# Kernel optimization log

Hardware: AMD Instinct MI355X
Metric: run time of the kernel (lower is better)

## Reference

```python
import jax, jax.numpy as jnp
import numpy as np

E, M, IN, OUT = 8, 8192, 2048, 8192


def setup_inputs() -> dict:
    key = jax.random.key(0)
    k1, k2, k3 = jax.random.split(key, 3)
    inputs = jax.random.normal(k1, (M, IN), dtype=jnp.float32)
    # truncated_normal(-3,3) scaled by init_scale/sqrt(In), matching MoELinear.init
    weight = jax.random.truncated_normal(k2, -3.0, 3.0, (E, IN, OUT), dtype=jnp.float32) * (1.0 / np.sqrt(IN))
    bias = jax.random.normal(k3, (OUT,), dtype=jnp.float32) * 0.02
    # tokens are pre-sorted by expert; balanced routing: M/E tokens per expert
    group_sizes = jnp.full((E,), M // E, dtype=jnp.int32)
    return {"inputs": inputs, "weight": weight, "group_sizes": group_sizes, "bias": bias}


def _ragged_matmul(inputs, weight, group_sizes):
    """Grouped GEMM: out[m] = inputs[m] @ weight[expert_of(m)].

    Tokens are contiguous per expert; group_sizes[e] gives the count for
    expert e. Same math as jax.lax.ragged_dot / megablox gmm.
    """
    n_experts = weight.shape[0]
    m = inputs.shape[0]
    # static-length repeat -> per-token expert id, jit-safe
    expert_ids = jnp.repeat(jnp.arange(n_experts, dtype=group_sizes.dtype),
                            group_sizes, total_repeat_length=m)  # [M]

    def body(acc, ew):
        e, w = ew  # w: [In, Out]
        mask = (expert_ids == e).astype(inputs.dtype)  # [M]
        return acc + (inputs * mask[:, None]) @ w, None

    acc0 = jnp.zeros((m, weight.shape[2]), dtype=inputs.dtype)
    out, _ = jax.lax.scan(body, acc0, (jnp.arange(n_experts, dtype=group_sizes.dtype), weight))
    return out


def reference(inputs, weight, group_sizes, bias):
    # MoELinear.__call__ (ragged_dot path): grouped matmul + bias
    return _ragged_matmul(inputs, weight, group_sizes) + bias
```

## Files before the change

### kernel.cpp

```cpp
#include <hip/hip_runtime.h>
#include <stdint.h>

#define E_ 8
#define M_ 8192
#define K_ 2048
#define N_ 8192

#define BM 256
#define BN 256
#define BK 64
#define NT (K_ / BK)
#define LDS_BYTES 131072

typedef __attribute__((ext_vector_type(8))) short bf16x8;
typedef __attribute__((ext_vector_type(4))) float f32x4;
typedef __attribute__((ext_vector_type(8))) unsigned short us8;

__device__ __forceinline__ unsigned short f2bf(float f) {
  union { float f; uint32_t u; } v; v.f = f;
  uint32_t u = v.u;
  uint32_t r = (u + 0x7FFFu + ((u >> 16) & 1u)) >> 16;
  return (unsigned short)r;
}

__device__ __forceinline__ void gload_lds16(const void* g, void* l) {
  __builtin_amdgcn_global_load_lds(
      (const __attribute__((address_space(1))) unsigned int*)g,
      (__attribute__((address_space(3))) unsigned int*)l,
      16, 0, 0);
}

__global__ __launch_bounds__(256) void conv_a(const float* __restrict__ A,
                                              unsigned short* __restrict__ Ab,
                                              int n8) {
  int stride = gridDim.x * blockDim.x;
  for (int idx = blockIdx.x * blockDim.x + threadIdx.x; idx < n8; idx += stride) {
    const float4* p = reinterpret_cast<const float4*>(A) + (size_t)idx * 2;
    float4 x0 = p[0], x1 = p[1];
    us8 o;
    o[0] = f2bf(x0.x); o[1] = f2bf(x0.y); o[2] = f2bf(x0.z); o[3] = f2bf(x0.w);
    o[4] = f2bf(x1.x); o[5] = f2bf(x1.y); o[6] = f2bf(x1.z); o[7] = f2bf(x1.w);
    *reinterpret_cast<us8*>(Ab + (size_t)idx * 8) = o;
  }
}

__global__ __launch_bounds__(256) void conv_wT(const float* __restrict__ W,
                                               unsigned short* __restrict__ Wt,
                                               int e_fixed) {
  __shared__ float t[64][65];
  int tid = threadIdx.x;
  int tx = tid & 63, ty = tid >> 6;
  int n0 = blockIdx.x * 64, k0 = blockIdx.y * 64;
  int e = (gridDim.z > 1) ? blockIdx.z : e_fixed;
  size_t win = (size_t)e * K_ * N_;
  size_t wout = (gridDim.z > 1) ? win : 0;

  #pragma unroll
  for (int r = 0; r < 16; ++r) {
    int kl = r * 4 + ty;
    t[kl][tx] = W[win + (size_t)(k0 + kl) * N_ + n0 + tx];
  }
  __syncthreads();
  int px = tid & 31, py = tid >> 5;
  #pragma unroll
  for (int r = 0; r < 8; ++r) {
    int nl = r * 8 + py;
    unsigned int pack = (unsigned int)f2bf(t[2 * px][nl]) |
                        ((unsigned int)f2bf(t[2 * px + 1][nl]) << 16);
    *reinterpret_cast<unsigned int*>(Wt + wout + (size_t)(n0 + nl) * K_ + k0 + 2 * px) = pack;
  }
}

__global__ __launch_bounds__(512, 2) void moe_gemm_bf16(
    const unsigned short* __restrict__ Ab,
    const unsigned short* __restrict__ Wt,
    const int* __restrict__ gs,
    const float* __restrict__ bias,
    float* __restrict__ C,
    int only_expert, size_t wt_stride) {
  extern __shared__ char smem[];

  int tile_n = blockIdx.x;
  int tile_m = blockIdx.y;

  int expert = -1, row_start = 0, rows = 0;
  if (only_expert >= 0) {
    int off = 0;
    for (int e = 0; e < only_expert; ++e) off += gs[e];
    int g = gs[only_expert];
    int t0 = tile_m * BM;
    if (t0 >= g) return;
    expert = only_expert;
    row_start = off + t0;
    rows = min(BM, g - t0);
  } else {
    int acc = 0, off = 0;
    for (int e = 0; e < E_; ++e) {
      int g = gs[e];
      int t = (g + BM - 1) / BM;
      if (expert < 0 && tile_m < acc + t) {
        int lt = tile_m - acc;
        expert = e;
        row_start = off + lt * BM;
        rows = min(BM, g - lt * BM);
      }
      acc += t;
      off += g;
    }
    if (expert < 0) return;
  }

  const unsigned short* WtE = Wt + (size_t)expert * wt_stride;

  int tid = threadIdx.x;
  int lane = tid & 63;
  int wave = tid >> 6;
  int wr = wave >> 2;
  int wc = wave & 3;
  int bh = wc >> 1;
  int ln15 = lane & 15;
  int n0 = tile_n * BN;

  int slot0 = (((lane >> 4) ^ (ln15 & 7)) << 4);
  int aBase = wr * 16384 + ln15 * 128;
  int bBase = 32768 + bh * 16384 + (wc & 1) * 8192 + ln15 * 128;

  int soff = tid * 16;
  int crow = tid >> 3;
  int lslot = (tid & 7) ^ (crow & 7);
  int scol = lslot * 8;

  const unsigned short* aS[4];
  const unsigned short* bS[4];
  #pragma unroll
  for (int c = 0; c < 4; ++c) {
    int r = c * 64 + crow;
    int gr = r < rows ? r : 0;
    aS[c] = Ab + (size_t)(row_start + gr) * K_ + scol;
    bS[c] = WtE + (size_t)(n0 + r) * K_ + scol;
  }

#define STG_A(DB, c, kt) \
  gload_lds16(aS[c] + (kt) * 64, smem + (DB) + (c) * 8192 + soff)
#define STG_B(DB, c, kt) \
  gload_lds16(bS[c] + (kt) * 64, smem + (DB) + 32768 + (c) * 8192 + soff)

  f32x4 acc4[8][4];
  #pragma unroll
  for (int i = 0; i < 8; ++i)
    #pragma unroll
    for (int j = 0; j < 4; ++j)
      acc4[i][j] = f32x4{0.f, 0.f, 0.f, 0.f};

#define DS_A(frag, DB, MH, KS)                                                \
  _Pragma("unroll") for (int mi = 0; mi < 4; ++mi)                            \
    frag[mi] = *(const bf16x8*)(smem + (DB) + aBase + (MH) * 8192 +           \
                                mi * 2048 + (slot0 ^ ((KS) << 6)));
#define DS_B(frag, DB, KS)                                                    \
  _Pragma("unroll") for (int nj = 0; nj < 4; ++nj)                            \
    frag[nj] = *(const bf16x8*)(smem + (DB) + bBase + nj * 2048 +             \
                                (slot0 ^ ((KS) << 6)));
#define MFMA16(MB, af, bf)                                                    \
  __builtin_amdgcn_s_setprio(1);                                              \
  _Pragma("unroll") for (int mi = 0; mi < 4; ++mi)                            \
    _Pragma("unroll") for (int nj = 0; nj < 4; ++nj)                          \
      acc4[(MB) + mi][nj] = __builtin_amdgcn_mfma_f32_16x16x32_bf16(          \
          af[mi], bf[nj], acc4[(MB) + mi][nj], 0, 0, 0);                      \
  __builtin_amdgcn_s_setprio(0);

#define TILE4(DB, DBN, KTN)                                                   \
  do {                                                                        \
    bf16x8 af[4], bf[4];                                                      \
                                                \
    DS_A(af, DB, 0, 0); DS_B(bf, DB, 0);                                      \
    STG_A(DBN, 0, KTN); STG_A(DBN, 2, KTN); STG_B(DBN, 0, KTN);               \
    __builtin_amdgcn_s_barrier();                                             \
    asm volatile("s_waitcnt lgkmcnt(0)" ::: "memory");                        \
    __builtin_amdgcn_sched_barrier(0);                                        \
    MFMA16(0, af, bf);                                                        \
    asm volatile("s_waitcnt vmcnt(3)" ::: "memory");                          \
    __builtin_amdgcn_s_barrier();                                             \
                             \
    DS_A(af, DB, 1, 0);                                                       \
    STG_B(DBN, 1, KTN); STG_B(DBN, 2, KTN); STG_B(DBN, 3, KTN);               \
    __builtin_amdgcn_s_barrier();                                             \
    asm volatile("s_waitcnt lgkmcnt(0)" ::: "memory");                        \
    __builtin_amdgcn_sched_barrier(0);                                        \
    MFMA16(4, af, bf);                                                        \
    __builtin_amdgcn_s_barrier();                                             \
                                                   \
    DS_A(af, DB, 0, 1); DS_B(bf, DB, 1);                                      \
    STG_A(DBN, 1, KTN); STG_A(DBN, 3, KTN);                                   \
    __builtin_amdgcn_s_barrier();                                             \
    asm volatile("s_waitcnt lgkmcnt(0)" ::: "memory");                        \
    __builtin_amdgcn_sched_barrier(0);                                        \
    MFMA16(0, af, bf);                                                        \
    __builtin_amdgcn_s_barrier();                                             \
                                                            \
    DS_A(af, DB, 1, 1);                                                       \
    __builtin_amdgcn_s_barrier();                                             \
    asm volatile("s_waitcnt lgkmcnt(0)" ::: "memory");                        \
    __builtin_amdgcn_sched_barrier(0);                                        \
    MFMA16(4, af, bf);                                                        \
    asm volatile("s_waitcnt vmcnt(2)" ::: "memory");                          \
    __builtin_amdgcn_s_barrier();                                             \
  } while (0)

  STG_B(0, 0, 0); STG_B(0, 1, 0); STG_B(0, 2, 0); STG_B(0, 3, 0);
  STG_A(0, 0, 0); STG_A(0, 2, 0);
  STG_A(0, 1, 0); STG_A(0, 3, 0);
  asm volatile("s_waitcnt vmcnt(2)" ::: "memory");
  __builtin_amdgcn_s_barrier();

  for (int t2 = 0; t2 < NT; t2 += 2) {
    int k2 = (t2 + 2 >= NT) ? 0 : t2 + 2;
    TILE4(0, 65536, t2 + 1);
    TILE4(65536, 0, k2);
  }
#undef TILE4
#undef DS_A
#undef DS_B
#undef MFMA16
#undef STG_A
#undef STG_B

  asm volatile("s_waitcnt vmcnt(0)" ::: "memory");

  float bv[4];
  #pragma unroll
  for (int nj = 0; nj < 4; ++nj) bv[nj] = bias[n0 + wc * 64 + nj * 16 + ln15];
  #pragma unroll
  for (int mi = 0; mi < 8; ++mi) {
    int r0 = wr * 128 + mi * 16 + (lane >> 4) * 4;
    #pragma unroll
    for (int r = 0; r < 4; ++r) {
      int lr = r0 + r;
      if (lr < rows) {
        float* Cp = C + (size_t)(row_start + lr) * N_ + n0 + wc * 64 + ln15;
        #pragma unroll
        for (int nj = 0; nj < 4; ++nj) Cp[nj * 16] = acc4[mi][nj][r] + bv[nj];
      }
    }
  }
}

__global__ __launch_bounds__(256) void moe_naive(const float* __restrict__ A,
                                                 const float* __restrict__ W,
                                                 const int* __restrict__ gs,
                                                 const float* __restrict__ bias,
                                                 float* __restrict__ C) {
  int col = blockIdx.x * 16 + (threadIdx.x & 15);
  int row = blockIdx.y * 16 + (threadIdx.x >> 4);
  int acc = 0, e = E_ - 1;
  for (int i = 0; i < E_; ++i) {
    int g = gs[i];
    if (row >= acc && row < acc + g) { e = i; break; }
    acc += g;
  }
  const float* a = A + (size_t)row * K_;
  const float* w = W + (size_t)e * K_ * N_ + col;
  float s = 0.f;
  for (int k = 0; k < K_; ++k) s += a[k] * w[(size_t)k * N_];
  C[(size_t)row * N_ + col] = s + bias[col];
}

extern "C" void kernel_launch(void* const* d_in, const int* in_sizes, int n_in,
                              void* d_out, int out_size, void* d_ws, size_t ws_size,
                              hipStream_t stream) {
  const float* A = (const float*)d_in[0];
  const float* W = (const float*)d_in[1];
  const int* gs = (const int*)d_in[2];
  const float* bias = (const float*)d_in[3];
  float* C = (float*)d_out;

  const size_t needA = (size_t)M_ * K_ * 2;
  const size_t needWall = (size_t)E_ * K_ * N_ * 2;
  const size_t needW1 = (size_t)K_ * N_ * 2;

  (void)hipFuncSetAttribute((const void*)moe_gemm_bf16,
                            hipFuncAttributeMaxDynamicSharedMemorySize, LDS_BYTES);

  if (ws_size >= needA + needWall) {
    unsigned short* Abf = (unsigned short*)d_ws;
    unsigned short* Wtb = (unsigned short*)((char*)d_ws + needA);
    conv_a<<<2048, 256, 0, stream>>>(A, Abf, (M_ * K_) / 8);
    dim3 gw(N_ / 64, K_ / 64, E_);
    conv_wT<<<gw, 256, 0, stream>>>(W, Wtb, 0);
    dim3 gg(N_ / BN, M_ / BM + E_);
    moe_gemm_bf16<<<gg, 512, LDS_BYTES, stream>>>(Abf, Wtb, gs, bias, C, -1, (size_t)N_ * K_);
  } else if (ws_size >= needA + needW1) {
    unsigned short* Abf = (unsigned short*)d_ws;
    unsigned short* Wtb = (unsigned short*)((char*)d_ws + needA);
    conv_a<<<2048, 256, 0, stream>>>(A, Abf, (M_ * K_) / 8);
    for (int e = 0; e < E_; ++e) {
      dim3 gw(N_ / 64, K_ / 64, 1);
      conv_wT<<<gw, 256, 0, stream>>>(W, Wtb, e);
      dim3 gg(N_ / BN, M_ / BM);
      moe_gemm_bf16<<<gg, 512, LDS_BYTES, stream>>>(Abf, Wtb, gs, bias, C, e, 0);
    }
  } else {
    dim3 gn(N_ / 16, M_ / 16);
    moe_naive<<<gn, 256, 0, stream>>>(A, W, gs, bias, C);
  }
}
```

Baseline: 431.2 us.

## Shrink GEMM tile to 128x128 with 4 waves and simplified pipeline

Reduces the block tile from 256x256 to 128x128, uses 256 threads and half the LDS, and each wave now owns a 64x64 output. Global-to-LDS staging is issued all at once per k-step and drained with a full vmcnt wait, replacing the staggered partial waits. The aim is higher occupancy and more blocks in the grid. In exchange, operand reuse per loaded byte drops and load latency is less hidden.

```diff
diff --git a/kernel.cpp b/kernel.cpp
--- a/kernel.cpp
+++ b/kernel.cpp
@@ -6,11 +6,12 @@
 #define K_ 2048
 #define N_ 8192
 
-#define BM 256
-#define BN 256
+#define BM 128
+#define BN 128
 #define BK 64
 #define NT (K_ / BK)
-#define LDS_BYTES 131072
+#define TILE_B 32768
+#define LDS_BYTES 65536
 
 typedef __attribute__((ext_vector_type(8))) short bf16x8;
 typedef __attribute__((ext_vector_type(4))) float f32x4;
@@ -71,7 +72,7 @@
   }
 }
 
-__global__ __launch_bounds__(512, 2) void moe_gemm_bf16(
+__global__ __launch_bounds__(256, 2) void moe_gemm_bf16(
     const unsigned short* __restrict__ Ab,
     const unsigned short* __restrict__ Wt,
     const int* __restrict__ gs,
@@ -115,15 +116,14 @@
   int tid = threadIdx.x;
   int lane = tid & 63;
   int wave = tid >> 6;
-  int wr = wave >> 2;
-  int wc = wave & 3;
-  int bh = wc >> 1;
+  int wr = wave >> 1;
+  int wc = wave & 1;
   int ln15 = lane & 15;
   int n0 = tile_n * BN;
 
   int slot0 = (((lane >> 4) ^ (ln15 & 7)) << 4);
-  int aBase = wr * 16384 + ln15 * 128;
-  int bBase = 32768 + bh * 16384 + (wc & 1) * 8192 + ln15 * 128;
+  int aBase = wr * 8192 + ln15 * 128;
+  int bBase = 16384 + wc * 8192 + ln15 * 128;
 
   int soff = tid * 16;
   int crow = tid >> 3;
@@ -134,104 +134,89 @@
   const unsigned short* bS[4];
   #pragma unroll
   for (int c = 0; c < 4; ++c) {
-    int r = c * 64 + crow;
+    int r = c * 32 + crow;
     int gr = r < rows ? r : 0;
     aS[c] = Ab + (size_t)(row_start + gr) * K_ + scol;
     bS[c] = WtE + (size_t)(n0 + r) * K_ + scol;
   }
 
 #define STG_A(DB, c, kt) \
-  gload_lds16(aS[c] + (kt) * 64, smem + (DB) + (c) * 8192 + soff)
+  gload_lds16(aS[c] + (kt) * 64, smem + (DB) + (c) * 4096 + soff)
 #define STG_B(DB, c, kt) \
-  gload_lds16(bS[c] + (kt) * 64, smem + (DB) + 32768 + (c) * 8192 + soff)
-
-  f32x4 acc4[8][4];
-  #pragma unroll
-  for (int i = 0; i < 8; ++i)
+  gload_lds16(bS[c] + (kt) * 64, smem + (DB) + 16384 + (c) * 4096 + soff)
+#define STG_ALL(DB, kt)                                                       \
+  do {                                                                        \
+    STG_B(DB, 0, kt); STG_B(DB, 1, kt); STG_B(DB, 2, kt); STG_B(DB, 3, kt);   \
+    STG_A(DB, 0, kt); STG_A(DB, 1, kt); STG_A(DB, 2, kt); STG_A(DB, 3, kt);   \
+  } while (0)
+
+  f32x4 acc4[4][4];
+  #pragma unroll
+  for (int i = 0; i < 4; ++i)
     #pragma unroll
     for (int j = 0; j < 4; ++j)
       acc4[i][j] = f32x4{0.f, 0.f, 0.f, 0.f};
 
-#define DS_A(frag, DB, MH, KS)                                                \
+#define DS_A(frag, DB, KS)                                                    \
   _Pragma("unroll") for (int mi = 0; mi < 4; ++mi)                            \
-    frag[mi] = *(const bf16x8*)(smem + (DB) + aBase + (MH) * 8192 +           \
-                                mi * 2048 + (slot0 ^ ((KS) << 6)));
+    frag[mi] = *(const bf16x8*)(smem + (DB) + aBase + mi * 2048 +             \
+                                (slot0 ^ ((KS) << 6)));
 #define DS_B(frag, DB, KS)                                                    \
   _Pragma("unroll") for (int nj = 0; nj < 4; ++nj)                            \
     frag[nj] = *(const bf16x8*)(smem + (DB) + bBase + nj * 2048 +             \
                                 (slot0 ^ ((KS) << 6)));
-#define MFMA16(MB, af, bf)                                                    \
+#define MFMA16(af, bf)                                                        \
   __builtin_amdgcn_s_setprio(1);                                              \
   _Pragma("unroll") for (int mi = 0; mi < 4; ++mi)                            \
     _Pragma("unroll") for (int nj = 0; nj < 4; ++nj)                          \
-      acc4[(MB) + mi][nj] = __builtin_amdgcn_mfma_f32_16x16x32_bf16(          \
-          af[mi], bf[nj], acc4[(MB) + mi][nj], 0, 0, 0);                      \
+      acc4[mi][nj] = __builtin_amdgcn_mfma_f32_16x16x32_bf16(                 \
+          af[mi], bf[nj], acc4[mi][nj], 0, 0, 0);                             \
   __builtin_amdgcn_s_setprio(0);
 
-#define TILE4(DB, DBN, KTN)                                                   \
+#define TILE2(DB, DBN, KTN)                                                   \
   do {                                                                        \
     bf16x8 af[4], bf[4];                                                      \
-                                                \
-    DS_A(af, DB, 0, 0); DS_B(bf, DB, 0);                                      \
-    STG_A(DBN, 0, KTN); STG_A(DBN, 2, KTN); STG_B(DBN, 0, KTN);               \
+                                                                      \
+    DS_A(af, DB, 0); DS_B(bf, DB, 0);                                         \
+    STG_ALL(DBN, KTN);                                                        \
     __builtin_amdgcn_s_barrier();                                             \
     asm volatile("s_waitcnt lgkmcnt(0)" ::: "memory");                        \
     __builtin_amdgcn_sched_barrier(0);                                        \
-    MFMA16(0, af, bf);                                                        \
-    asm volatile("s_waitcnt vmcnt(3)" ::: "memory");                          \
-    __builtin_amdgcn_s_barrier();                                             \
-                             \
-    DS_A(af, DB, 1, 0);                                                       \
-    STG_B(DBN, 1, KTN); STG_B(DBN, 2, KTN); STG_B(DBN, 3, KTN);               \
+    MFMA16(af, bf);                                                           \
+    __builtin_amdgcn_s_barrier();                                             \
+                                                                      \
+    DS_A(af, DB, 1); DS_B(bf, DB, 1);                                         \
     __builtin_amdgcn_s_barrier();                                             \
     asm volatile("s_waitcnt lgkmcnt(0)" ::: "memory");                        \
     __builtin_amdgcn_sched_barrier(0);                                        \
-    MFMA16(4, af, bf);                                                        \
-    __builtin_amdgcn_s_barrier();                                             \
-                                                   \
-    DS_A(af, DB, 0, 1); DS_B(bf, DB, 1);                                      \
-    STG_A(DBN, 1, KTN); STG_A(DBN, 3, KTN);                                   \
-    __builtin_amdgcn_s_barrier();                                             \
-    asm volatile("s_waitcnt lgkmcnt(0)" ::: "memory");                        \
-    __builtin_amdgcn_sched_barrier(0);                                        \
-    MFMA16(0, af, bf);                                                        \
-    __builtin_amdgcn_s_barrier();                                             \
-                                                            \
-    DS_A(af, DB, 1, 1);                                                       \
-    __builtin_amdgcn_s_barrier();                                             \
-    asm volatile("s_waitcnt lgkmcnt(0)" ::: "memory");                        \
-    __builtin_amdgcn_sched_barrier(0);                                        \
-    MFMA16(4, af, bf);                                                        \
-    asm volatile("s_waitcnt vmcnt(2)" ::: "memory");                          \
+    MFMA16(af, bf);                                                           \
+    asm volatile("s_waitcnt vmcnt(0)" ::: "memory");                          \
     __builtin_amdgcn_s_barrier();                                             \
   } while (0)
 
-  STG_B(0, 0, 0); STG_B(0, 1, 0); STG_B(0, 2, 0); STG_B(0, 3, 0);
-  STG_A(0, 0, 0); STG_A(0, 2, 0);
-  STG_A(0, 1, 0); STG_A(0, 3, 0);
-  asm volatile("s_waitcnt vmcnt(2)" ::: "memory");
+  STG_ALL(0, 0);
+  asm volatile("s_waitcnt vmcnt(0)" ::: "memory");
   __builtin_amdgcn_s_barrier();
 
   for (int t2 = 0; t2 < NT; t2 += 2) {
     int k2 = (t2 + 2 >= NT) ? 0 : t2 + 2;
-    TILE4(0, 65536, t2 + 1);
-    TILE4(65536, 0, k2);
-  }
-#undef TILE4
+    TILE2(0, TILE_B, t2 + 1);
+    TILE2(TILE_B, 0, k2);
+  }
+#undef TILE2
 #undef DS_A
 #undef DS_B
 #undef MFMA16
 #undef STG_A
 #undef STG_B
-
-  asm volatile("s_waitcnt vmcnt(0)" ::: "memory");
+#undef STG_ALL
 
   float bv[4];
   #pragma unroll
   for (int nj = 0; nj < 4; ++nj) bv[nj] = bias[n0 + wc * 64 + nj * 16 + ln15];
   #pragma unroll
-  for (int mi = 0; mi < 8; ++mi) {
-    int r0 = wr * 128 + mi * 16 + (lane >> 4) * 4;
+  for (int mi = 0; mi < 4; ++mi) {
+    int r0 = wr * 64 + mi * 16 + (lane >> 4) * 4;
     #pragma unroll
     for (int r = 0; r < 4; ++r) {
       int lr = r0 + r;
@@ -287,7 +272,7 @@
     dim3 gw(N_ / 64, K_ / 64, E_);
     conv_wT<<<gw, 256, 0, stream>>>(W, Wtb, 0);
     dim3 gg(N_ / BN, M_ / BM + E_);
-    moe_gemm_bf16<<<gg, 512, LDS_BYTES, stream>>>(Abf, Wtb, gs, bias, C, -1, (size_t)N_ * K_);
+    moe_gemm_bf16<<<gg, 256, LDS_BYTES, stream>>>(Abf, Wtb, gs, bias, C, -1, (size_t)N_ * K_);
   } else if (ws_size >= needA + needW1) {
     unsigned short* Abf = (unsigned short*)d_ws;
     unsigned short* Wtb = (unsigned short*)((char*)d_ws + needA);
@@ -296,7 +281,7 @@
       dim3 gw(N_ / 64, K_ / 64, 1);
       conv_wT<<<gw, 256, 0, stream>>>(W, Wtb, e);
       dim3 gg(N_ / BN, M_ / BM);
-      moe_gemm_bf16<<<gg, 512, LDS_BYTES, stream>>>(Abf, Wtb, gs, bias, C, e, 0);
+      moe_gemm_bf16<<<gg, 256, LDS_BYTES, stream>>>(Abf, Wtb, gs, bias, C, e, 0);
     }
   } else {
     dim3 gn(N_ / 16, M_ / 16);
```

After: 484.8 us. 1.12x slower.

## Replace four-phase interleaved K-tile schedule with single-phase issue-all-then-compute loop

Applied to the files above, without the earlier changes.

Drops the hand-interleaved four-phase schedule, which split global-to-LDS staging and MFMA work across several barriers per K tile. Each tile now issues all eight next-tile loads up front, runs all MFMAs from the current LDS buffer with compiler-scheduled LDS reads, then waits on all loads and synchronises once. The aim is to cut barrier count and waitcnt stalls. In exchange, LDS reads are no longer explicitly separated from MFMAs, and the full vmcnt(0) wait per tile may expose load latency.

```diff
diff --git a/kernel.cpp b/kernel.cpp
--- a/kernel.cpp
+++ b/kernel.cpp
@@ -144,6 +144,11 @@
   gload_lds16(aS[c] + (kt) * 64, smem + (DB) + (c) * 8192 + soff)
 #define STG_B(DB, c, kt) \
   gload_lds16(bS[c] + (kt) * 64, smem + (DB) + 32768 + (c) * 8192 + soff)
+#define STG_ALL(DB, kt)                                                       \
+  do {                                                                        \
+    STG_B(DB, 0, kt); STG_B(DB, 1, kt); STG_B(DB, 2, kt); STG_B(DB, 3, kt);   \
+    STG_A(DB, 0, kt); STG_A(DB, 1, kt); STG_A(DB, 2, kt); STG_A(DB, 3, kt);   \
+  } while (0)
 
   f32x4 acc4[8][4];
   #pragma unroll
@@ -152,79 +157,45 @@
     for (int j = 0; j < 4; ++j)
       acc4[i][j] = f32x4{0.f, 0.f, 0.f, 0.f};
 
-#define DS_A(frag, DB, MH, KS)                                                \
-  _Pragma("unroll") for (int mi = 0; mi < 4; ++mi)                            \
-    frag[mi] = *(const bf16x8*)(smem + (DB) + aBase + (MH) * 8192 +           \
-                                mi * 2048 + (slot0 ^ ((KS) << 6)));
-#define DS_B(frag, DB, KS)                                                    \
-  _Pragma("unroll") for (int nj = 0; nj < 4; ++nj)                            \
-    frag[nj] = *(const bf16x8*)(smem + (DB) + bBase + nj * 2048 +             \
-                                (slot0 ^ ((KS) << 6)));
-#define MFMA16(MB, af, bf)                                                    \
-  __builtin_amdgcn_s_setprio(1);                                              \
-  _Pragma("unroll") for (int mi = 0; mi < 4; ++mi)                            \
-    _Pragma("unroll") for (int nj = 0; nj < 4; ++nj)                          \
-      acc4[(MB) + mi][nj] = __builtin_amdgcn_mfma_f32_16x16x32_bf16(          \
-          af[mi], bf[nj], acc4[(MB) + mi][nj], 0, 0, 0);                      \
-  __builtin_amdgcn_s_setprio(0);
-
-#define TILE4(DB, DBN, KTN)                                                   \
+#define TILE1(DB, DBN, KTN)                                                   \
   do {                                                                        \
-    bf16x8 af[4], bf[4];                                                      \
-                                                \
-    DS_A(af, DB, 0, 0); DS_B(bf, DB, 0);                                      \
-    STG_A(DBN, 0, KTN); STG_A(DBN, 2, KTN); STG_B(DBN, 0, KTN);               \
-    __builtin_amdgcn_s_barrier();                                             \
-    asm volatile("s_waitcnt lgkmcnt(0)" ::: "memory");                        \
-    __builtin_amdgcn_sched_barrier(0);                                        \
-    MFMA16(0, af, bf);                                                        \
-    asm volatile("s_waitcnt vmcnt(3)" ::: "memory");                          \
-    __builtin_amdgcn_s_barrier();                                             \
-                             \
-    DS_A(af, DB, 1, 0);                                                       \
-    STG_B(DBN, 1, KTN); STG_B(DBN, 2, KTN); STG_B(DBN, 3, KTN);               \
-    __builtin_amdgcn_s_barrier();                                             \
-    asm volatile("s_waitcnt lgkmcnt(0)" ::: "memory");                        \
-    __builtin_amdgcn_sched_barrier(0);                                        \
-    MFMA16(4, af, bf);                                                        \
-    __builtin_amdgcn_s_barrier();                                             \
-                                                   \
-    DS_A(af, DB, 0, 1); DS_B(bf, DB, 1);                                      \
-    STG_A(DBN, 1, KTN); STG_A(DBN, 3, KTN);                                   \
-    __builtin_amdgcn_s_barrier();                                             \
-    asm volatile("s_waitcnt lgkmcnt(0)" ::: "memory");                        \
-    __builtin_amdgcn_sched_barrier(0);                                        \
-    MFMA16(0, af, bf);                                                        \
-    __builtin_amdgcn_s_barrier();                                             \
-                                                            \
-    DS_A(af, DB, 1, 1);                                                       \
-    __builtin_amdgcn_s_barrier();                                             \
-    asm volatile("s_waitcnt lgkmcnt(0)" ::: "memory");                        \
-    __builtin_amdgcn_sched_barrier(0);                                        \
-    MFMA16(4, af, bf);                                                        \
-    asm volatile("s_waitcnt vmcnt(2)" ::: "memory");                          \
+    STG_ALL(DBN, KTN);                                                        \
+    __builtin_amdgcn_sched_barrier(0);                 \
+    __builtin_amdgcn_s_setprio(1);                                            \
+    _Pragma("unroll") for (int ks = 0; ks < 2; ++ks) {                        \
+      bf16x8 bfr[4];                                                          \
+      _Pragma("unroll") for (int nj = 0; nj < 4; ++nj)                        \
+        bfr[nj] = *(const bf16x8*)(smem + (DB) + bBase + nj * 2048 +          \
+                                   (slot0 ^ (ks << 6)));                      \
+      _Pragma("unroll") for (int mh = 0; mh < 2; ++mh) {                      \
+        bf16x8 afr[4];                                                        \
+        _Pragma("unroll") for (int mi = 0; mi < 4; ++mi)                      \
+          afr[mi] = *(const bf16x8*)(smem + (DB) + aBase + mh * 8192 +        \
+                                     mi * 2048 + (slot0 ^ (ks << 6)));        \
+        _Pragma("unroll") for (int mi = 0; mi < 4; ++mi)                      \
+          _Pragma("unroll") for (int nj = 0; nj < 4; ++nj)                    \
+            acc4[mh * 4 + mi][nj] = __builtin_amdgcn_mfma_f32_16x16x32_bf16(  \
+                afr[mi], bfr[nj], acc4[mh * 4 + mi][nj], 0, 0, 0);            \
+      }                                                                       \
+    }                                                                         \
+    __builtin_amdgcn_s_setprio(0);                                            \
+    asm volatile("s_waitcnt vmcnt(0)" ::: "memory");                          \
     __builtin_amdgcn_s_barrier();                                             \
   } while (0)
 
-  STG_B(0, 0, 0); STG_B(0, 1, 0); STG_B(0, 2, 0); STG_B(0, 3, 0);
-  STG_A(0, 0, 0); STG_A(0, 2, 0);
-  STG_A(0, 1, 0); STG_A(0, 3, 0);
-  asm volatile("s_waitcnt vmcnt(2)" ::: "memory");
+  STG_ALL(0, 0);
+  asm volatile("s_waitcnt vmcnt(0)" ::: "memory");
   __builtin_amdgcn_s_barrier();
 
   for (int t2 = 0; t2 < NT; t2 += 2) {
     int k2 = (t2 + 2 >= NT) ? 0 : t2 + 2;
-    TILE4(0, 65536, t2 + 1);
-    TILE4(65536, 0, k2);
-  }
-#undef TILE4
-#undef DS_A
-#undef DS_B
-#undef MFMA16
+    TILE1(0, 65536, t2 + 1);
+    TILE1(65536, 0, k2);
+  }
+#undef TILE1
 #undef STG_A
 #undef STG_B
-
-  asm volatile("s_waitcnt vmcnt(0)" ::: "memory");
+#undef STG_ALL
 
   float bv[4];
   #pragma unroll
```

New measurement: 439.3 us. About the same (+1.9%).
